# Optimization experiments

Measured on AMD Instinct MI355X. Metric: run time of the kernel, lower is better.

The kernel has to match this reference:

```python
import jax, jax.numpy as jnp
import numpy as np

TOKENS = 8192
IN_F = 4096
OUT_F = 4096
ZERO_POINT = 0  # int8 activation zero point (module default)


def setup_inputs() -> dict:
    key = jax.random.key(0)
    k1, k2, k3, k4 = jax.random.split(key, 4)
    # int8-valued activations/weights stored as int32 (same math as torch upcast path)
    x = jax.random.randint(k1, (TOKENS, IN_F), 0, 127, dtype=jnp.int32)
    weight = jax.random.randint(k2, (IN_F, OUT_F), -127, 127, dtype=jnp.int32)
    bias = jax.random.randint(k3, (1, OUT_F), -64, 64, dtype=jnp.int32)
    gemm_scales = jax.random.uniform(k4, (1, OUT_F), dtype=jnp.float32) * 1e-3
    return {"x": x, "weight": weight, "bias": bias, "gemm_scales": gemm_scales}


def reference(x, weight, bias, gemm_scales):
    # adjust_a = (x - zero_point), upcast to float32 like the torch module
    adjust_a = (x - ZERO_POINT).astype(jnp.float32)          # [T, in]
    w = weight.astype(jnp.float32)                           # [in, out]
    gemm_o = (adjust_a @ w + bias.astype(jnp.float32)) * gemm_scales  # [T, out]
    return gemm_o
```

## Files before the change

kernel.cpp:

```cpp
#include <hip/hip_runtime.h>

using i32x4 = __attribute__((ext_vector_type(4))) int;

#define AS3(p) ((__attribute__((address_space(3))) void*)(p))
#define AS1(p) ((const __attribute__((address_space(1))) void*)(p))

constexpr int M = 8192;
constexpr int N = 4096;
constexpr int K = 4096;

__global__ void pack_a_kernel(const int4* __restrict__ x, unsigned* __restrict__ a8, int nUnits) {
    int stride = gridDim.x * blockDim.x;
    for (int u = blockIdx.x * blockDim.x + threadIdx.x; u < nUnits; u += stride) {
        int4 v = x[u];
        a8[u] = (v.x & 255) | ((v.y & 255) << 8) | ((v.z & 255) << 16) | (v.w << 24);
    }
}

__global__ void pack_wT_kernel(const int* __restrict__ w, char* __restrict__ b8t) {
    __shared__ __align__(16) char T[64][80];
    const int n0 = blockIdx.x * 64;
    const int k0 = blockIdx.y * 64;
    const int tid = threadIdx.x;

    #pragma unroll
    for (int i = 0; i < 4; i++) {
        int u = tid + i * 256;
        int r = u >> 4;
        int c = u & 15;
        int4 v = *(const int4*)&w[(size_t)(k0 + r) * N + n0 + 4 * c];
        T[4 * c + 0][r] = (char)v.x;
        T[4 * c + 1][r] = (char)v.y;
        T[4 * c + 2][r] = (char)v.z;
        T[4 * c + 3][r] = (char)v.w;
    }
    __syncthreads();

    const int n = tid >> 2;
    const int q = tid & 3;
    int4 val = *(const int4*)&T[n][16 * q];
    *(int4*)&b8t[(size_t)(n0 + n) * K + k0 + 16 * q] = val;
}

__global__ __launch_bounds__(512, 2) void gemm_i8_kernel(
    const char* __restrict__ a8, const char* __restrict__ b8t,
    const int* __restrict__ bias, const float* __restrict__ scales,
    float* __restrict__ out)
{
    __shared__ __align__(16) char As[2][256 * 64];
    __shared__ __align__(16) char Bs[2][256 * 64];

    const int tid  = threadIdx.x;
    const int lane = tid & 63;
    const int wid  = tid >> 6;
    const int wr   = wid >> 2;
    const int wc   = wid & 3;

    const int bid = blockIdx.x;
    const int cpx = gridDim.x >> 3;
    const int sw  = (bid & 7) * cpx + (bid >> 3);
    const int tm  = sw >> 4;
    const int tn  = sw & 15;
    const size_t brow = (size_t)tm * 256;
    const size_t bcol = (size_t)tn * 256;

    const int srow = tid >> 2;
    const int sch  = (tid & 3) << 4;
    const char* aG = a8  + (brow + srow) * (size_t)K + sch;
    const char* bG = b8t + (bcol + srow) * (size_t)K + sch;
    const int ldsOff = wid * 1024;

    i32x4 acc[8][4];
    #pragma unroll
    for (int m = 0; m < 8; m++)
        #pragma unroll
        for (int n = 0; n < 4; n++)
            #pragma unroll
            for (int r = 0; r < 4; r++)
                acc[m][n][r] = 0;

    auto stage = [&](int buf, int kt) {
        const char* ak = aG + kt * 64;
        const char* bk = bG + kt * 64;
        __builtin_amdgcn_global_load_lds(AS1(ak),                    AS3(&As[buf][ldsOff]),        16, 0, 0);
        __builtin_amdgcn_global_load_lds(AS1(ak + (size_t)128 * K),  AS3(&As[buf][8192 + ldsOff]), 16, 0, 0);
        __builtin_amdgcn_global_load_lds(AS1(bk),                    AS3(&Bs[buf][ldsOff]),        16, 0, 0);
        __builtin_amdgcn_global_load_lds(AS1(bk + (size_t)128 * K),  AS3(&Bs[buf][8192 + ldsOff]), 16, 0, 0);
    };

    stage(0, 0);
    __syncthreads();

    const int rowoff = (lane & 15) * 64 + (lane >> 4) * 16;

    int cur = 0;
    for (int kt = 0; kt < K / 64; kt++) {
        if (kt + 1 < K / 64) stage(cur ^ 1, kt + 1);

        const char* Ab = &As[cur][wr * 8192];
        const char* Bb = &Bs[cur][wc * 4096];
        i32x4 bfr[4];
        #pragma unroll
        for (int n = 0; n < 4; n++)
            bfr[n] = *(const i32x4*)(Bb + n * 1024 + rowoff);
        #pragma unroll
        for (int m = 0; m < 8; m++) {
            i32x4 afr = *(const i32x4*)(Ab + m * 1024 + rowoff);
            #pragma unroll
            for (int n = 0; n < 4; n++)
                acc[m][n] = __builtin_amdgcn_mfma_i32_16x16x64_i8(afr, bfr[n], acc[m][n], 0, 0, 0);
        }
        __syncthreads();
        cur ^= 1;
    }

    #pragma unroll
    for (int n = 0; n < 4; n++) {
        const int col = (int)bcol + wc * 64 + n * 16 + (lane & 15);
        const int bv  = bias[col];
        const float sv = scales[col];
        #pragma unroll
        for (int m = 0; m < 8; m++) {
            const size_t row0 = brow + wr * 128 + m * 16 + ((lane >> 4) << 2);
            float* o = out + row0 * (size_t)N + col;
            #pragma unroll
            for (int r = 0; r < 4; r++)
                o[(size_t)r * N] = (float)(acc[m][n][r] + bv) * sv;
        }
    }
}

extern "C" void kernel_launch(void* const* d_in, const int* in_sizes, int n_in,
                              void* d_out, int out_size, void* d_ws, size_t ws_size,
                              hipStream_t stream) {
    const int*   x      = (const int*)d_in[0];
    const int*   w      = (const int*)d_in[1];
    const int*   bias   = (const int*)d_in[2];
    const float* scales = (const float*)d_in[3];
    float* out = (float*)d_out;

    char* a8  = (char*)d_ws;
    char* b8t = a8 + (size_t)M * K;

    pack_a_kernel<<<2048, 256, 0, stream>>>((const int4*)x, (unsigned*)a8, M * K / 4);

    dim3 gt(N / 64, K / 64);
    pack_wT_kernel<<<gt, 256, 0, stream>>>(w, b8t);

    gemm_i8_kernel<<<(M / 256) * (N / 256), 512, 0, stream>>>(a8, b8t, bias, scales, out);
}
```

Baseline: 239.2 us.

## Double K tile to 128 with XOR-swizzled LDS and phased MFMA schedule

Raises the K tile from 64 to 128 bytes, XOR-swizzles the LDS column chunks to avoid bank conflicts, and splits each K step into four phases with explicit barriers, waitcnts, sched_barriers and setprio around MFMA bursts. The goal is fewer loop iterations and barriers per K, conflict-free fragment reads, and better overlap of global-to-LDS prefetch with MFMA work. The LDS footprint doubles to 128 KB, so launch bounds drop to one block per SM, which lowers occupancy and leans harder on the hand-written schedule.

```diff
diff --git a/kernel.cpp b/kernel.cpp
--- a/kernel.cpp
+++ b/kernel.cpp
@@ -8,6 +8,8 @@
 constexpr int M = 8192;
 constexpr int N = 4096;
 constexpr int K = 4096;
+constexpr int BK = 128;
+constexpr int NT = K / BK;
 
 __global__ void pack_a_kernel(const int4* __restrict__ x, unsigned* __restrict__ a8, int nUnits) {
     int stride = gridDim.x * blockDim.x;
@@ -42,13 +44,13 @@
     *(int4*)&b8t[(size_t)(n0 + n) * K + k0 + 16 * q] = val;
 }
 
-__global__ __launch_bounds__(512, 2) void gemm_i8_kernel(
+__global__ __launch_bounds__(512, 1) void gemm_i8_kernel(
     const char* __restrict__ a8, const char* __restrict__ b8t,
     const int* __restrict__ bias, const float* __restrict__ scales,
     float* __restrict__ out)
 {
-    __shared__ __align__(16) char As[2][256 * 64];
-    __shared__ __align__(16) char Bs[2][256 * 64];
+    __shared__ __align__(16) char As[2][256 * BK];
+    __shared__ __align__(16) char Bs[2][256 * BK];
 
     const int tid  = threadIdx.x;
     const int lane = tid & 63;
@@ -64,11 +66,11 @@
     const size_t brow = (size_t)tm * 256;
     const size_t bcol = (size_t)tn * 256;
 
-    const int srow = tid >> 2;
-    const int sch  = (tid & 3) << 4;
-    const char* aG = a8  + (brow + srow) * (size_t)K + sch;
-    const char* bG = b8t + (bcol + srow) * (size_t)K + sch;
-    const int ldsOff = wid * 1024;
+    const int srow = tid >> 3;
+    const int schS = ((tid & 7) ^ (srow & 7)) << 4;
+    const char* aG = a8  + (brow + srow) * (size_t)K + schS;
+    const char* bG = b8t + (bcol + srow) * (size_t)K + schS;
+    const int ldsW = wid * 1024;
 
     i32x4 acc[8][4];
     #pragma unroll
@@ -79,52 +81,103 @@
             for (int r = 0; r < 4; r++)
                 acc[m][n][r] = 0;
 
-    auto stage = [&](int buf, int kt) {
-        const char* ak = aG + kt * 64;
-        const char* bk = bG + kt * 64;
-        __builtin_amdgcn_global_load_lds(AS1(ak),                    AS3(&As[buf][ldsOff]),        16, 0, 0);
-        __builtin_amdgcn_global_load_lds(AS1(ak + (size_t)128 * K),  AS3(&As[buf][8192 + ldsOff]), 16, 0, 0);
-        __builtin_amdgcn_global_load_lds(AS1(bk),                    AS3(&Bs[buf][ldsOff]),        16, 0, 0);
-        __builtin_amdgcn_global_load_lds(AS1(bk + (size_t)128 * K),  AS3(&Bs[buf][8192 + ldsOff]), 16, 0, 0);
+    auto stageAll = [&](int b, int kt) {
+        const char* a  = aG + (size_t)kt * BK;
+        const char* bb = bG + (size_t)kt * BK;
+        char* Ad = &As[b][0] + ldsW;
+        char* Bd = &Bs[b][0] + ldsW;
+        __builtin_amdgcn_global_load_lds(AS1(a),                  AS3(Ad),         16, 0, 0);
+        __builtin_amdgcn_global_load_lds(AS1(a  + (size_t) 64*K), AS3(Ad +  8192), 16, 0, 0);
+        __builtin_amdgcn_global_load_lds(AS1(a  + (size_t)128*K), AS3(Ad + 16384), 16, 0, 0);
+        __builtin_amdgcn_global_load_lds(AS1(a  + (size_t)192*K), AS3(Ad + 24576), 16, 0, 0);
+        __builtin_amdgcn_global_load_lds(AS1(bb),                 AS3(Bd),         16, 0, 0);
+        __builtin_amdgcn_global_load_lds(AS1(bb + (size_t) 64*K), AS3(Bd +  8192), 16, 0, 0);
+        __builtin_amdgcn_global_load_lds(AS1(bb + (size_t)128*K), AS3(Bd + 16384), 16, 0, 0);
+        __builtin_amdgcn_global_load_lds(AS1(bb + (size_t)192*K), AS3(Bd + 24576), 16, 0, 0);
     };
 
-    stage(0, 0);
-    __syncthreads();
-
-    const int rowoff = (lane & 15) * 64 + (lane >> 4) * 16;
+    const int frow = lane & 15;
+    const int c0 = ((lane >> 4) ^ (lane & 7)) << 4;
+    const int c1 = c0 ^ 64;
+    const int raBase = wr * 16384 + frow * 128;
+    const int rbBase = wc * 8192  + frow * 128;
+
+    stageAll(0, 0);
+    asm volatile("s_waitcnt vmcnt(0)" ::: "memory");
+    __builtin_amdgcn_s_barrier();
 
     int cur = 0;
-    for (int kt = 0; kt < K / 64; kt++) {
-        if (kt + 1 < K / 64) stage(cur ^ 1, kt + 1);
-
-        const char* Ab = &As[cur][wr * 8192];
-        const char* Bb = &Bs[cur][wc * 4096];
-        i32x4 bfr[4];
-        #pragma unroll
-        for (int n = 0; n < 4; n++)
-            bfr[n] = *(const i32x4*)(Bb + n * 1024 + rowoff);
-        #pragma unroll
-        for (int m = 0; m < 8; m++) {
-            i32x4 afr = *(const i32x4*)(Ab + m * 1024 + rowoff);
-            #pragma unroll
-            for (int n = 0; n < 4; n++)
-                acc[m][n] = __builtin_amdgcn_mfma_i32_16x16x64_i8(afr, bfr[n], acc[m][n], 0, 0, 0);
-        }
-        __syncthreads();
+    for (int kt = 0; kt < NT; ++kt) {
+        const char* Ab = &As[cur][0] + raBase;
+        const char* Bb = &Bs[cur][0] + rbBase;
+
+        i32x4 bfr[4][2];
+
+        if (kt + 1 < NT) stageAll(cur ^ 1, kt + 1);
+        #pragma unroll
+        for (int n = 0; n < 4; ++n) {
+            bfr[n][0] = *(const i32x4*)(Bb + n * 2048 + c0);
+            bfr[n][1] = *(const i32x4*)(Bb + n * 2048 + c1);
+        }
+        {
+            i32x4 a00 = *(const i32x4*)(Ab + 0 * 2048 + c0);
+            i32x4 a01 = *(const i32x4*)(Ab + 0 * 2048 + c1);
+            i32x4 a10 = *(const i32x4*)(Ab + 1 * 2048 + c0);
+            i32x4 a11 = *(const i32x4*)(Ab + 1 * 2048 + c1);
+            __builtin_amdgcn_s_barrier();
+            asm volatile("s_waitcnt lgkmcnt(0)" ::: "memory");
+            __builtin_amdgcn_sched_barrier(0);
+            __builtin_amdgcn_s_setprio(1);
+            #pragma unroll
+            for (int n = 0; n < 4; ++n) {
+                acc[0][n] = __builtin_amdgcn_mfma_i32_16x16x64_i8(a00, bfr[n][0], acc[0][n], 0, 0, 0);
+                acc[0][n] = __builtin_amdgcn_mfma_i32_16x16x64_i8(a01, bfr[n][1], acc[0][n], 0, 0, 0);
+                acc[1][n] = __builtin_amdgcn_mfma_i32_16x16x64_i8(a10, bfr[n][0], acc[1][n], 0, 0, 0);
+                acc[1][n] = __builtin_amdgcn_mfma_i32_16x16x64_i8(a11, bfr[n][1], acc[1][n], 0, 0, 0);
+            }
+            __builtin_amdgcn_s_setprio(0);
+            __builtin_amdgcn_sched_barrier(0);
+            __builtin_amdgcn_s_barrier();
+        }
+
+        #pragma unroll
+        for (int p = 1; p < 4; ++p) {
+            i32x4 a00 = *(const i32x4*)(Ab + (2 * p)     * 2048 + c0);
+            i32x4 a01 = *(const i32x4*)(Ab + (2 * p)     * 2048 + c1);
+            i32x4 a10 = *(const i32x4*)(Ab + (2 * p + 1) * 2048 + c0);
+            i32x4 a11 = *(const i32x4*)(Ab + (2 * p + 1) * 2048 + c1);
+            __builtin_amdgcn_s_barrier();
+            asm volatile("s_waitcnt lgkmcnt(0)" ::: "memory");
+            __builtin_amdgcn_sched_barrier(0);
+            __builtin_amdgcn_s_setprio(1);
+            #pragma unroll
+            for (int n = 0; n < 4; ++n) {
+                acc[2 * p][n]     = __builtin_amdgcn_mfma_i32_16x16x64_i8(a00, bfr[n][0], acc[2 * p][n], 0, 0, 0);
+                acc[2 * p][n]     = __builtin_amdgcn_mfma_i32_16x16x64_i8(a01, bfr[n][1], acc[2 * p][n], 0, 0, 0);
+                acc[2 * p + 1][n] = __builtin_amdgcn_mfma_i32_16x16x64_i8(a10, bfr[n][0], acc[2 * p + 1][n], 0, 0, 0);
+                acc[2 * p + 1][n] = __builtin_amdgcn_mfma_i32_16x16x64_i8(a11, bfr[n][1], acc[2 * p + 1][n], 0, 0, 0);
+            }
+            __builtin_amdgcn_s_setprio(0);
+            __builtin_amdgcn_sched_barrier(0);
+            if (p == 3) {
+                asm volatile("s_waitcnt vmcnt(0)" ::: "memory");
+            }
+            __builtin_amdgcn_s_barrier();
+        }
         cur ^= 1;
     }
 
     #pragma unroll
-    for (int n = 0; n < 4; n++) {
+    for (int n = 0; n < 4; ++n) {
         const int col = (int)bcol + wc * 64 + n * 16 + (lane & 15);
         const int bv  = bias[col];
         const float sv = scales[col];
         #pragma unroll
-        for (int m = 0; m < 8; m++) {
+        for (int m = 0; m < 8; ++m) {
             const size_t row0 = brow + wr * 128 + m * 16 + ((lane >> 4) << 2);
             float* o = out + row0 * (size_t)N + col;
             #pragma unroll
-            for (int r = 0; r < 4; r++)
+            for (int r = 0; r < 4; ++r)
                 o[(size_t)r * N] = (float)(acc[m][n][r] + bv) * sv;
         }
     }
```

New measurement: 225.5 us. -5.8%, faster.

## Deepen GEMM pipeline to four LDS stages with swizzle and manual waitcnt scheduling

Applied to the files above, without the earlier changes.

Replaces the double-buffered main loop of the int8 GEMM with a 4-slot ring that keeps three tiles of global→LDS loads in flight, gated by explicit vmcnt/lgkmcnt waits and raw s_barrier calls instead of __syncthreads. Adds an XOR swizzle on the 16-byte chunk index to reduce LDS bank conflicts on fragment reads, splits the MFMA work into two halves with setprio and sched_barrier so the second half overlaps the remaining LDS reads, and changes the block-to-tile mapping so each XCD covers a contiguous 8x8 tile region. The doubled LDS footprint forces one block per CU (launch bounds lowered), which trades occupancy for deeper prefetch.

```diff
diff --git a/kernel.cpp b/kernel.cpp
--- a/kernel.cpp
+++ b/kernel.cpp
@@ -8,6 +8,9 @@
 constexpr int M = 8192;
 constexpr int N = 4096;
 constexpr int K = 4096;
+constexpr int BK = 64;
+constexpr int NT = K / BK;
+constexpr int NBUF = 4;
 
 __global__ void pack_a_kernel(const int4* __restrict__ x, unsigned* __restrict__ a8, int nUnits) {
     int stride = gridDim.x * blockDim.x;
@@ -42,13 +45,13 @@
     *(int4*)&b8t[(size_t)(n0 + n) * K + k0 + 16 * q] = val;
 }
 
-__global__ __launch_bounds__(512, 2) void gemm_i8_kernel(
+__global__ __launch_bounds__(512, 1) void gemm_i8_kernel(
     const char* __restrict__ a8, const char* __restrict__ b8t,
     const int* __restrict__ bias, const float* __restrict__ scales,
     float* __restrict__ out)
 {
-    __shared__ __align__(16) char As[2][256 * 64];
-    __shared__ __align__(16) char Bs[2][256 * 64];
+    __shared__ __align__(16) char As[NBUF][256 * BK];
+    __shared__ __align__(16) char Bs[NBUF][256 * BK];
 
     const int tid  = threadIdx.x;
     const int lane = tid & 63;
@@ -57,18 +60,18 @@
     const int wc   = wid & 3;
 
     const int bid = blockIdx.x;
-    const int cpx = gridDim.x >> 3;
-    const int sw  = (bid & 7) * cpx + (bid >> 3);
-    const int tm  = sw >> 4;
-    const int tn  = sw & 15;
+    const int xcd = bid & 7;
+    const int l   = bid >> 3;
+    const int tm  = (xcd >> 1) * 8 + (l >> 3);
+    const int tn  = (xcd & 1) * 8 + (l & 7);
     const size_t brow = (size_t)tm * 256;
     const size_t bcol = (size_t)tn * 256;
 
     const int srow = tid >> 2;
-    const int sch  = (tid & 3) << 4;
-    const char* aG = a8  + (brow + srow) * (size_t)K + sch;
-    const char* bG = b8t + (bcol + srow) * (size_t)K + sch;
-    const int ldsOff = wid * 1024;
+    const int schS = ((tid & 3) ^ ((tid >> 3) & 3)) << 4;
+    const char* aG = a8  + (brow + srow) * (size_t)K + schS;
+    const char* bG = b8t + (bcol + srow) * (size_t)K + schS;
+    const int ldsW = wid * 1024;
 
     i32x4 acc[8][4];
     #pragma unroll
@@ -79,52 +82,84 @@
             for (int r = 0; r < 4; r++)
                 acc[m][n][r] = 0;
 
-    auto stage = [&](int buf, int kt) {
-        const char* ak = aG + kt * 64;
-        const char* bk = bG + kt * 64;
-        __builtin_amdgcn_global_load_lds(AS1(ak),                    AS3(&As[buf][ldsOff]),        16, 0, 0);
-        __builtin_amdgcn_global_load_lds(AS1(ak + (size_t)128 * K),  AS3(&As[buf][8192 + ldsOff]), 16, 0, 0);
-        __builtin_amdgcn_global_load_lds(AS1(bk),                    AS3(&Bs[buf][ldsOff]),        16, 0, 0);
-        __builtin_amdgcn_global_load_lds(AS1(bk + (size_t)128 * K),  AS3(&Bs[buf][8192 + ldsOff]), 16, 0, 0);
+    auto stage = [&](int slot, int kt) {
+        const char* a = aG + (size_t)kt * BK;
+        const char* b = bG + (size_t)kt * BK;
+        char* Ad = &As[slot][0] + ldsW;
+        char* Bd = &Bs[slot][0] + ldsW;
+        __builtin_amdgcn_global_load_lds(AS1(a),                  AS3(Ad),        16, 0, 0);
+        __builtin_amdgcn_global_load_lds(AS1(a + (size_t)128*K),  AS3(Ad + 8192), 16, 0, 0);
+        __builtin_amdgcn_global_load_lds(AS1(b),                  AS3(Bd),        16, 0, 0);
+        __builtin_amdgcn_global_load_lds(AS1(b + (size_t)128*K),  AS3(Bd + 8192), 16, 0, 0);
     };
 
+    const int frow  = lane & 15;
+    const int c0sw  = ((lane >> 4) ^ ((frow >> 1) & 3)) << 4;
+    const int raOff = wr * 8192 + frow * 64 + c0sw;
+    const int rbOff = wc * 4096 + frow * 64 + c0sw;
+
     stage(0, 0);
-    __syncthreads();
+    stage(1, 1);
+    stage(2, 2);
+    asm volatile("s_waitcnt vmcnt(8)" ::: "memory");
+    __builtin_amdgcn_s_barrier();
 
-    const int rowoff = (lane & 15) * 64 + (lane >> 4) * 16;
+    #pragma unroll 4
+    for (int t = 0; t < NT; ++t) {
+        const int slot = t & 3;
+        if (t + 3 < NT) stage((t + 3) & 3, t + 3);
 
-    int cur = 0;
-    for (int kt = 0; kt < K / 64; kt++) {
-        if (kt + 1 < K / 64) stage(cur ^ 1, kt + 1);
+        const char* Ab = &As[slot][0] + raOff;
+        const char* Bb = &Bs[slot][0] + rbOff;
 
-        const char* Ab = &As[cur][wr * 8192];
-        const char* Bb = &Bs[cur][wc * 4096];
-        i32x4 bfr[4];
+        i32x4 bfr[4], afr[8];
         #pragma unroll
-        for (int n = 0; n < 4; n++)
-            bfr[n] = *(const i32x4*)(Bb + n * 1024 + rowoff);
+        for (int n = 0; n < 4; ++n)
+            bfr[n] = *(const i32x4*)(Bb + n * 1024);
         #pragma unroll
-        for (int m = 0; m < 8; m++) {
-            i32x4 afr = *(const i32x4*)(Ab + m * 1024 + rowoff);
+        for (int m = 0; m < 8; ++m)
+            afr[m] = *(const i32x4*)(Ab + m * 1024);
+
+        __builtin_amdgcn_s_barrier();
+
+        asm volatile("s_waitcnt lgkmcnt(4)" ::: "memory");
+        __builtin_amdgcn_sched_barrier(0);
+        __builtin_amdgcn_s_setprio(1);
+        #pragma unroll
+        for (int m = 0; m < 4; ++m)
             #pragma unroll
-            for (int n = 0; n < 4; n++)
-                acc[m][n] = __builtin_amdgcn_mfma_i32_16x16x64_i8(afr, bfr[n], acc[m][n], 0, 0, 0);
-        }
-        __syncthreads();
-        cur ^= 1;
+            for (int n = 0; n < 4; ++n)
+                acc[m][n] = __builtin_amdgcn_mfma_i32_16x16x64_i8(afr[m], bfr[n], acc[m][n], 0, 0, 0);
+        __builtin_amdgcn_s_setprio(0);
+        __builtin_amdgcn_sched_barrier(0);
+
+        asm volatile("s_waitcnt lgkmcnt(0)" ::: "memory");
+        __builtin_amdgcn_sched_barrier(0);
+        __builtin_amdgcn_s_setprio(1);
+        #pragma unroll
+        for (int m = 4; m < 8; ++m)
+            #pragma unroll
+            for (int n = 0; n < 4; ++n)
+                acc[m][n] = __builtin_amdgcn_mfma_i32_16x16x64_i8(afr[m], bfr[n], acc[m][n], 0, 0, 0);
+        __builtin_amdgcn_s_setprio(0);
+        __builtin_amdgcn_sched_barrier(0);
+
+        if (t <= NT - 4) asm volatile("s_waitcnt vmcnt(8)" ::: "memory");
+        else             asm volatile("s_waitcnt vmcnt(0)" ::: "memory");
+        __builtin_amdgcn_s_barrier();
     }
 
     #pragma unroll
-    for (int n = 0; n < 4; n++) {
+    for (int n = 0; n < 4; ++n) {
         const int col = (int)bcol + wc * 64 + n * 16 + (lane & 15);
         const int bv  = bias[col];
         const float sv = scales[col];
         #pragma unroll
-        for (int m = 0; m < 8; m++) {
+        for (int m = 0; m < 8; ++m) {
             const size_t row0 = brow + wr * 128 + m * 16 + ((lane >> 4) << 2);
             float* o = out + row0 * (size_t)N + col;
             #pragma unroll
-            for (int r = 0; r < 4; r++)
+            for (int r = 0; r < 4; ++r)
                 o[(size_t)r * N] = (float)(acc[m][n][r] + bv) * sv;
         }
     }
```

After: 206.4 us. -13.7%, faster.
